# Performance work log

Measured on AMD Instinct MI355X. Metric: run time of the kernel, lower is better.

## Reference

```python
import jax, jax.numpy as jnp
import numpy as np

TOPK = 13
NUM_CLASSES = 80
ALPHA = 1.0
BETA = 6.0
EPS = 1e-9
IMG = 640.0


def setup_inputs() -> dict:
    key = jax.random.key(0)
    k = jax.random.split(key, 8)
    bs, A, C, n = 32, 8400, NUM_CLASSES, 64
    pd_scores = jax.random.uniform(k[0], (bs, A, C), dtype=jnp.float32)
    # valid x1y1x2y2 predicted boxes
    ctr = jax.random.uniform(k[1], (bs, A, 2), dtype=jnp.float32) * IMG
    wh = jax.random.uniform(k[2], (bs, A, 2), dtype=jnp.float32) * 90.0 + 10.0
    pd_bboxes = jnp.concatenate([ctr - wh / 2, ctr + wh / 2], axis=-1)
    anc_points = jax.random.uniform(k[3], (8400, 2), dtype=jnp.float32) * IMG
    gt_labels = jax.random.randint(k[4], (bs, n, 1), 0, C, dtype=jnp.int64)
    gctr = jax.random.uniform(k[5], (bs, n, 2), dtype=jnp.float32) * IMG
    gwh = jax.random.uniform(k[6], (bs, n, 2), dtype=jnp.float32) * 140.0 + 20.0
    gt_bboxes = jnp.concatenate([gctr - gwh / 2, gctr + gwh / 2], axis=-1)
    mask_gt = (jax.random.uniform(k[7], (bs, n, 1)) < 0.8).astype(jnp.float32)
    return {"pd_scores": pd_scores, "pd_bboxes": pd_bboxes, "anc_points": anc_points,
            "gt_labels": gt_labels, "gt_bboxes": gt_bboxes, "mask_gt": mask_gt}


def _assign(pd_scores, pd_bboxes, anc_points, gt_labels, gt_bboxes, mask_gt):
    b, A, C = pd_scores.shape
    n = gt_bboxes.shape[1]
    gl = gt_labels.reshape(b, n).astype(jnp.int32)

    # bbox_scores[b,n,a] = pd_scores[b, a, gt_labels[b,n]]  -> (b, n, A)
    bbox_scores = jnp.take_along_axis(pd_scores.transpose(0, 2, 1), gl[:, :, None], axis=1)

    # pairwise IoU: gt (b,n,1,4) vs pred (b,1,A,4) -> (b,n,A)
    b1 = gt_bboxes[:, :, None, :]
    b2 = pd_bboxes[:, None, :, :]
    lt = jnp.maximum(b1[..., :2], b2[..., :2])
    rb = jnp.minimum(b1[..., 2:], b2[..., 2:])
    overlap = jnp.clip(rb - lt, 0).prod(-1)
    area1 = jnp.clip(b1[..., 2:] - b1[..., :2], 0).prod(-1)
    area2 = jnp.clip(b2[..., 2:] - b2[..., :2], 0).prod(-1)
    overlaps = overlap / (area1 + area2 - overlap + EPS)

    align_metric = (bbox_scores ** ALPHA) * (overlaps ** BETA)

    # anchor centers inside gt boxes -> (b,n,A)
    lt_d = anc_points[None, None, :, :] - gt_bboxes[:, :, None, :2]
    rb_d = gt_bboxes[:, :, None, 2:] - anc_points[None, None, :, :]
    deltas = jnp.concatenate([lt_d, rb_d], axis=-1)
    mask_in_gts = (deltas.min(-1) > EPS).astype(gt_bboxes.dtype)

    # topk candidate selection with scatter-count (avoids (b,n,topk,A) one-hot)
    metrics = align_metric * mask_in_gts
    _, topk_idxs = jax.lax.top_k(metrics, TOPK)  # (b,n,TOPK)
    topk_mask = mask_gt.reshape(b, n, 1) != 0
    topk_idxs = jnp.where(topk_mask, topk_idxs, 0)
    bi = jnp.arange(b)[:, None, None]
    ni = jnp.arange(n)[None, :, None]
    counts = jnp.zeros((b, n, A), jnp.int32).at[bi, ni, topk_idxs].add(1)
    is_in_topk = jnp.where(counts > 1, 0, counts).astype(metrics.dtype)

    mask_pos = is_in_topk * mask_in_gts * mask_gt.reshape(b, n, 1)

    # resolve anchors assigned to multiple gts by highest IoU
    fg_mask = mask_pos.sum(-2)                         # (b,A)
    mask_multi = fg_mask[:, None, :] > 1               # (b,1,A) broadcast over n
    max_idx = overlaps.argmax(axis=1)                  # (b,A)
    is_max = jax.nn.one_hot(max_idx, n, dtype=overlaps.dtype).transpose(0, 2, 1)  # (b,n,A)
    mask_pos = jnp.where(mask_multi, is_max, mask_pos)
    fg_mask = mask_pos.sum(-2)
    target_gt_idx = mask_pos.argmax(-2)                # (b,A)

    # gather targets
    target_labels = jnp.take_along_axis(gl, target_gt_idx, axis=1)            # (b,A)
    target_labels = jnp.maximum(target_labels, 0)
    target_bboxes = jnp.take_along_axis(gt_bboxes, target_gt_idx[:, :, None], axis=1)  # (b,A,4)
    target_scores = jax.nn.one_hot(target_labels, C, dtype=pd_scores.dtype)
    target_scores = jnp.where(fg_mask[:, :, None] > 0, target_scores, 0.0)

    # normalize scores by alignment metric
    align_metric = align_metric * mask_pos
    pos_align = align_metric.max(-1, keepdims=True)                  # (b,n,1)
    pos_overlaps = (overlaps * mask_pos).max(-1, keepdims=True)      # (b,n,1)
    norm = (align_metric * pos_overlaps / (pos_align + EPS)).max(-2)[:, :, None]  # (b,A,1)
    target_scores = target_scores * norm

    return target_labels, target_bboxes, target_scores, fg_mask > 0


def reference(pd_scores, pd_bboxes, anc_points, gt_labels, gt_bboxes, mask_gt):
    return _assign(pd_scores, pd_bboxes, anc_points, gt_labels, gt_bboxes, mask_gt)
```

## Files before the change

### kernel.cpp

```cpp
#include <hip/hip_runtime.h>
#include <math.h>

#define A_N   8400
#define BS    32
#define NGT   64
#define NC    80
#define TK    13
#define EPSF  1e-9f
#define CAP   1024
#define JG    32
#define NJG   2
#define NTILE 33
#define PCAP  64

typedef float nt4 __attribute__((ext_vector_type(4)));

#define OFF_LB 0
#define OFF_BB (BS * A_N)
#define OFF_SC (OFF_BB + BS * A_N * 4)
#define OFF_FG (OFF_SC + BS * A_N * NC)

#define WS_FLAG   0
#define WS_CNT    256
#define WS_MINJ   (WS_CNT   + BS * A_N * 4)
#define WS_INFO   (WS_MINJ  + BS * A_N * 4)
#define WS_ALIGN  (WS_INFO  + BS * A_N * 4)
#define WS_POSA   (WS_ALIGN + BS * A_N * 4)
#define WS_POSO   (WS_POSA  + BS * NGT * 4)
#define WS_CNT2   (WS_POSO  + BS * NGT * 4)
#define WS_CAND   (WS_CNT2  + BS * NGT * 4)

__device__ __forceinline__ float iou_f(float g0, float g1, float g2, float g3,
                                       float p0, float p1, float p2, float p3) {
    float ltx = fmaxf(g0, p0), lty = fmaxf(g1, p1);
    float rbx = fminf(g2, p2), rby = fminf(g3, p3);
    float ov  = fmaxf(rbx - ltx, 0.f) * fmaxf(rby - lty, 0.f);
    float a1  = fmaxf(g2 - g0, 0.f) * fmaxf(g3 - g1, 0.f);
    float a2  = fmaxf(p2 - p0, 0.f) * fmaxf(p3 - p1, 0.f);
    return ov / (a1 + a2 - ov + EPSF);
}

__device__ __forceinline__ int get_gl(const int* g, int flag64, int i) {
    return flag64 ? g[2 * i] : g[i];
}

__device__ __forceinline__ unsigned long long shfl_xor_u64(unsigned long long x, int m) {
    int lo = __shfl_xor((int)(unsigned int)(x & 0xFFFFFFFFull), m, 64);
    int hi = __shfl_xor((int)(unsigned int)(x >> 32), m, 64);
    return ((unsigned long long)(unsigned int)hi << 32) | (unsigned int)lo;
}

__global__ __launch_bounds__(256) void k_init(int* cnt, int* minj,
                                              unsigned int* posA, unsigned int* posO,
                                              int* cnt2, int* flag, const int* gl_raw) {
    int i = blockIdx.x * 256 + threadIdx.x;
    if (i < BS * A_N) { cnt[i] = 0; minj[i] = 1 << 30; }
    if (i < BS * NGT) { posA[i] = 0u; posO[i] = 0u; cnt2[i] = 0; }
    if (i == 0) {
        int f = 1;
        for (int k = 0; k < 64; k++) {
            if (gl_raw[2 * k + 1] != 0) { f = 0; break; }
        }
        *flag = f;
    }
}

__global__ __launch_bounds__(256) void k_cand(
    const float* __restrict__ pd_scores, const float* __restrict__ pd_bboxes,
    const float* __restrict__ anc, const int* __restrict__ gl_raw,
    const float* __restrict__ gt_bboxes, const float* __restrict__ mask_gt,
    const int* __restrict__ flag,
    int* __restrict__ cnt2, unsigned long long* __restrict__ cand) {
    __shared__ float4 sgt[JG];
    __shared__ int    slbl[JG];
    __shared__ int    smask[JG];
    __shared__ int    cnt_lds[JG];
    __shared__ int    base_lds[JG];
    __shared__ unsigned long long pool[JG][PCAP];

    int bid  = blockIdx.x;
    int b    = bid / (NTILE * NJG);
    int rem  = bid % (NTILE * NJG);
    int tile = rem / NJG;
    int jg   = rem % NJG;
    int tid  = threadIdx.x;
    int a    = tile * 256 + tid;
    int jbase = b * NGT + jg * JG;

    if (tid < JG) {
        sgt[tid]   = ((const float4*)gt_bboxes)[jbase + tid];
        slbl[tid]  = get_gl(gl_raw, *flag, jbase + tid);
        smask[tid] = (mask_gt[jbase + tid] != 0.f);
        cnt_lds[tid] = 0;
    }
    __syncthreads();

    bool act = (a < A_N);
    float2 an = make_float2(0.f, 0.f);
    float4 p  = make_float4(0.f, 0.f, 0.f, 0.f);
    const float* sc = pd_scores;
    if (act) {
        an = ((const float2*)anc)[a];
        p  = ((const float4*)pd_bboxes)[(size_t)b * A_N + a];
        sc = pd_scores + (size_t)b * A_N * NC + (size_t)a * NC;
    }

    for (int j = 0; j < JG; j++) {
        if (!smask[j]) continue;
        if (!act) continue;
        float4 g = sgt[j];
        float d = fminf(fminf(an.x - g.x, an.y - g.y),
                        fminf(g.z - an.x, g.w - an.y));
        if (d > EPSF) {
            float iou = iou_f(g.x, g.y, g.z, g.w, p.x, p.y, p.z, p.w);
            float m = 0.f;
            if (iou > 0.f) {
                float s = sc[slbl[j]];
                m = s * powf(iou, 6.0f);
            }
            unsigned long long key =
                ((unsigned long long)__float_as_uint(m) << 32) |
                (unsigned int)(~(unsigned int)a);
            int slot = atomicAdd(&cnt_lds[j], 1);
            if (slot < PCAP) {
                pool[j][slot] = key;
            } else {
                int gs = atomicAdd(&cnt2[jbase + j], 1);
                if (gs < CAP) cand[(size_t)(jbase + j) * CAP + gs] = key;
            }
        }
    }
    __syncthreads();

    if (tid < JG) {
        int c = min(cnt_lds[tid], PCAP);
        int bas = 0;
        if (c > 0) bas = atomicAdd(&cnt2[jbase + tid], c);
        base_lds[tid] = bas;
    }
    __syncthreads();

    for (int j = 0; j < JG; j++) {
        int c = min(cnt_lds[j], PCAP);
        int bas = base_lds[j];
        for (int t = tid; t < c; t += 256) {
            int dst = bas + t;
            if (dst < CAP) cand[(size_t)(jbase + j) * CAP + dst] = pool[j][t];
        }
    }
}

__global__ __launch_bounds__(256) void k_pick(
    const int* __restrict__ cnt2, const unsigned long long* __restrict__ cand,
    int* __restrict__ cnt, int* __restrict__ minj) {
    int lane = threadIdx.x & 63;
    int wave = threadIdx.x >> 6;
    int bj = blockIdx.x * 4 + wave;
    int b = bj >> 6, j = bj & 63;

    int n = min(cnt2[bj], CAP);
    if (n == 0) return;

    const unsigned long long* L = cand + (size_t)bj * CAP;
    unsigned long long k0[CAP / 64];
    #pragma unroll
    for (int t = 0; t < CAP / 64; t++) {
        int i = t * 64 + lane;
        k0[t] = (i < n) ? L[i] : 0ULL;
    }

    unsigned int wanchor[TK];
    int P = 0;
    #pragma unroll
    for (int r = 0; r < TK; r++) {
        unsigned long long best = 0;
        #pragma unroll
        for (int t = 0; t < CAP / 64; t++) best = (k0[t] > best) ? k0[t] : best;
        for (int s = 1; s < 64; s <<= 1) {
            unsigned long long o = shfl_xor_u64(best, s);
            if (o > best) best = o;
        }
        if (!(best >> 32)) break;
        unsigned int aw = ~(unsigned int)(best & 0xFFFFFFFFull);
        wanchor[r] = aw;
        if (lane == 0) {
            atomicAdd(&cnt[b * A_N + (int)aw], 1);
            atomicMin(&minj[b * A_N + (int)aw], j);
        }
        #pragma unroll
        for (int t = 0; t < CAP / 64; t++) if (k0[t] == best) k0[t] = 0;
        P++;
    }

    if (P < TK) {
        int K = TK - P;
        #pragma unroll
        for (int t = 0; t < CAP / 64; t++) {
            unsigned long long key = k0[t];
            if (key != 0 && !(key >> 32)) {
                unsigned int a0 = ~(unsigned int)(key & 0xFFFFFFFFull);
                int off = 0;
                #pragma unroll
                for (int r = 0; r < TK; r++)
                    if (r < P && wanchor[r] < a0) off++;
                if ((int)a0 < K + off) {
                    atomicAdd(&cnt[b * A_N + (int)a0], 1);
                    atomicMin(&minj[b * A_N + (int)a0], j);
                }
            }
        }
    }
}

__global__ __launch_bounds__(256) void k_assign(
    const float* __restrict__ pd_scores, const float* __restrict__ pd_bboxes,
    const float* __restrict__ gt_bboxes, const int* __restrict__ gl_raw,
    const int* __restrict__ flag,
    const int* __restrict__ cnt, const int* __restrict__ minj,
    int* __restrict__ info, float* __restrict__ alignArr,
    unsigned int* posA, unsigned int* posO, float* __restrict__ out) {
    int i = blockIdx.x * 256 + threadIdx.x;
    if (i >= BS * A_N) return;
    int b = i / A_N;
    int c = cnt[i];
    int f64 = *flag;

    float4 p = ((const float4*)pd_bboxes)[i];
    int jstar = 0;
    if (c == 1) {
        jstar = minj[i];
    } else if (c > 1) {
        float bv = -1.f; int bj_ = 0;
        const float4* gb = (const float4*)(gt_bboxes + (size_t)b * NGT * 4);
        for (int j = 0; j < NGT; j++) {
            float4 g = gb[j];
            float ov = iou_f(g.x, g.y, g.z, g.w, p.x, p.y, p.z, p.w);
            if (ov > bv) { bv = ov; bj_ = j; }
        }
        jstar = bj_;
    }

    int lbl = get_gl(gl_raw, f64, b * NGT + jstar);
    if (lbl < 0) lbl = 0;

    out[OFF_LB + i] = (float)lbl;
    float4 g = ((const float4*)gt_bboxes)[b * NGT + jstar];
    ((float4*)(out + OFF_BB))[i] = g;

    int fg = (c > 0) ? 1 : 0;
    out[OFF_FG + i] = (float)fg;

    float al = 0.f;
    if (fg) {
        float ov = iou_f(g.x, g.y, g.z, g.w, p.x, p.y, p.z, p.w);
        float s  = pd_scores[(size_t)i * NC + lbl];
        al = s * powf(ov, 6.0f);
        atomicMax((int*)&posA[b * NGT + jstar], __float_as_int(al));
        atomicMax((int*)&posO[b * NGT + jstar], __float_as_int(ov));
    }
    alignArr[i] = al;
    info[i] = jstar | (lbl << 8) | (fg << 16);
}

__global__ __launch_bounds__(256) void k_scores(
    const int* __restrict__ info, const float* __restrict__ alignArr,
    const unsigned int* __restrict__ posA, const unsigned int* __restrict__ posO,
    float* __restrict__ out) {
    int t = blockIdx.x * 256 + threadIdx.x;
    const int TOT = BS * A_N * (NC / 4);
    if (t >= TOT) return;
    int anchor = t / (NC / 4);
    int q = t - anchor * (NC / 4);
    int inf = info[anchor];
    nt4 v = (nt4)(0.f);
    if (inf & (1 << 16)) {
        int lbl = (inf >> 8) & 255;
        int c0 = q * 4;
        if (lbl >= c0 && lbl < c0 + 4) {
            int jstar = inf & 255;
            int b = anchor / A_N;
            float pa = __int_as_float((int)posA[b * NGT + jstar]);
            float po = __int_as_float((int)posO[b * NGT + jstar]);
            float norm = alignArr[anchor] * po / (pa + EPSF);
            v[lbl - c0] = norm;
        }
    }
    __builtin_nontemporal_store(v, &((nt4*)(out + OFF_SC))[t]);
}

extern "C" void kernel_launch(void* const* d_in, const int* in_sizes, int n_in,
                              void* d_out, int out_size, void* d_ws, size_t ws_size,
                              hipStream_t stream) {
    const float* pd_scores = (const float*)d_in[0];
    const float* pd_bboxes = (const float*)d_in[1];
    const float* anc       = (const float*)d_in[2];
    const int*   gl_raw    = (const int*)d_in[3];
    const float* gt_bboxes = (const float*)d_in[4];
    const float* mask_gt   = (const float*)d_in[5];
    float* out = (float*)d_out;

    char* ws = (char*)d_ws;
    int*                flag     = (int*)(ws + WS_FLAG);
    int*                cnt      = (int*)(ws + WS_CNT);
    int*                minj     = (int*)(ws + WS_MINJ);
    int*                info     = (int*)(ws + WS_INFO);
    float*              alignArr = (float*)(ws + WS_ALIGN);
    unsigned int*       posA     = (unsigned int*)(ws + WS_POSA);
    unsigned int*       posO     = (unsigned int*)(ws + WS_POSO);
    int*                cnt2     = (int*)(ws + WS_CNT2);
    unsigned long long* cand     = (unsigned long long*)(ws + WS_CAND);

    k_init<<<(BS * A_N + 255) / 256, 256, 0, stream>>>(cnt, minj, posA, posO, cnt2, flag, gl_raw);
    k_cand<<<BS * NTILE * NJG, 256, 0, stream>>>(pd_scores, pd_bboxes, anc, gl_raw,
                                                 gt_bboxes, mask_gt, flag, cnt2, cand);
    k_pick<<<BS * NGT / 4, 256, 0, stream>>>(cnt2, cand, cnt, minj);
    k_assign<<<(BS * A_N + 255) / 256, 256, 0, stream>>>(pd_scores, pd_bboxes, gt_bboxes,
                                                         gl_raw, flag, cnt, minj,
                                                         info, alignArr, posA, posO, out);
    k_scores<<<(BS * A_N * (NC / 4) + 255) / 256, 256, 0, stream>>>(info, alignArr,
                                                                    posA, posO, out);
}
```

Baseline: 217.3 us.

## Zero score output inside candidate kernel and scatter only positive norms

The dense zero fill of the score output and the cnt/minj initialisation move into k_cand as grid-stride loops, so they overlap with the candidate computation and k_init shrinks to a tiny launch. The final kernel now writes a single scalar per foreground anchor instead of rewriting the whole 80-class row. This removes a full pass that read info per vec4 and wrote the dense score tensor. In exchange k_cand carries extra store traffic, and the ordering between the zero fill and the later scattered writes relies on kernel boundaries.

Measured after the change: 215.7 us. About the same (-0.8%).

```diff
diff --git a/kernel.cpp b/kernel.cpp
--- a/kernel.cpp
+++ b/kernel.cpp
@@ -12,6 +12,7 @@
 #define NJG   2
 #define NTILE 33
 #define PCAP  64
+#define NCAND (BS * NTILE * NJG)
 
 typedef float nt4 __attribute__((ext_vector_type(4)));
 
@@ -50,11 +51,9 @@
     return ((unsigned long long)(unsigned int)hi << 32) | (unsigned int)lo;
 }
 
-__global__ __launch_bounds__(256) void k_init(int* cnt, int* minj,
-                                              unsigned int* posA, unsigned int* posO,
+__global__ __launch_bounds__(256) void k_init(unsigned int* posA, unsigned int* posO,
                                               int* cnt2, int* flag, const int* gl_raw) {
     int i = blockIdx.x * 256 + threadIdx.x;
-    if (i < BS * A_N) { cnt[i] = 0; minj[i] = 1 << 30; }
     if (i < BS * NGT) { posA[i] = 0u; posO[i] = 0u; cnt2[i] = 0; }
     if (i == 0) {
         int f = 1;
@@ -70,7 +69,8 @@
     const float* __restrict__ anc, const int* __restrict__ gl_raw,
     const float* __restrict__ gt_bboxes, const float* __restrict__ mask_gt,
     const int* __restrict__ flag,
-    int* __restrict__ cnt2, unsigned long long* __restrict__ cand) {
+    int* __restrict__ cnt2, unsigned long long* __restrict__ cand,
+    int* __restrict__ cnt, int* __restrict__ minj, float* __restrict__ out) {
     __shared__ float4 sgt[JG];
     __shared__ int    slbl[JG];
     __shared__ int    smask[JG];
@@ -92,6 +92,17 @@
         slbl[tid]  = get_gl(gl_raw, *flag, jbase + tid);
         smask[tid] = (mask_gt[jbase + tid] != 0.f);
         cnt_lds[tid] = 0;
+    }
+
+    {
+        int gth = bid * 256 + tid;
+        const int GS = NCAND * 256;
+        nt4* scz = (nt4*)(out + OFF_SC);
+        for (int t = gth; t < BS * A_N * (NC / 4); t += GS)
+            __builtin_nontemporal_store((nt4)(0.f), &scz[t]);
+        for (int t = gth; t < BS * A_N; t += GS) {
+            cnt[t] = 0; minj[t] = 1 << 30;
+        }
     }
     __syncthreads();
 
@@ -262,30 +273,20 @@
     info[i] = jstar | (lbl << 8) | (fg << 16);
 }
 
-__global__ __launch_bounds__(256) void k_scores(
+__global__ __launch_bounds__(256) void k_norm(
     const int* __restrict__ info, const float* __restrict__ alignArr,
     const unsigned int* __restrict__ posA, const unsigned int* __restrict__ posO,
     float* __restrict__ out) {
-    int t = blockIdx.x * 256 + threadIdx.x;
-    const int TOT = BS * A_N * (NC / 4);
-    if (t >= TOT) return;
-    int anchor = t / (NC / 4);
-    int q = t - anchor * (NC / 4);
-    int inf = info[anchor];
-    nt4 v = (nt4)(0.f);
-    if (inf & (1 << 16)) {
-        int lbl = (inf >> 8) & 255;
-        int c0 = q * 4;
-        if (lbl >= c0 && lbl < c0 + 4) {
-            int jstar = inf & 255;
-            int b = anchor / A_N;
-            float pa = __int_as_float((int)posA[b * NGT + jstar]);
-            float po = __int_as_float((int)posO[b * NGT + jstar]);
-            float norm = alignArr[anchor] * po / (pa + EPSF);
-            v[lbl - c0] = norm;
-        }
-    }
-    __builtin_nontemporal_store(v, &((nt4*)(out + OFF_SC))[t]);
+    int i = blockIdx.x * 256 + threadIdx.x;
+    if (i >= BS * A_N) return;
+    int inf = info[i];
+    if (!(inf & (1 << 16))) return;
+    int jstar = inf & 255;
+    int lbl   = (inf >> 8) & 255;
+    int b = i / A_N;
+    float pa = __int_as_float((int)posA[b * NGT + jstar]);
+    float po = __int_as_float((int)posO[b * NGT + jstar]);
+    out[OFF_SC + (size_t)i * NC + lbl] = alignArr[i] * po / (pa + EPSF);
 }
 
 extern "C" void kernel_launch(void* const* d_in, const int* in_sizes, int n_in,
@@ -310,13 +311,13 @@
     int*                cnt2     = (int*)(ws + WS_CNT2);
     unsigned long long* cand     = (unsigned long long*)(ws + WS_CAND);
 
-    k_init<<<(BS * A_N + 255) / 256, 256, 0, stream>>>(cnt, minj, posA, posO, cnt2, flag, gl_raw);
-    k_cand<<<BS * NTILE * NJG, 256, 0, stream>>>(pd_scores, pd_bboxes, anc, gl_raw,
-                                                 gt_bboxes, mask_gt, flag, cnt2, cand);
+    k_init<<<8, 256, 0, stream>>>(posA, posO, cnt2, flag, gl_raw);
+    k_cand<<<NCAND, 256, 0, stream>>>(pd_scores, pd_bboxes, anc, gl_raw,
+                                      gt_bboxes, mask_gt, flag, cnt2, cand,
+                                      cnt, minj, out);
     k_pick<<<BS * NGT / 4, 256, 0, stream>>>(cnt2, cand, cnt, minj);
     k_assign<<<(BS * A_N + 255) / 256, 256, 0, stream>>>(pd_scores, pd_bboxes, gt_bboxes,
                                                          gl_raw, flag, cnt, minj,
                                                          info, alignArr, posA, posO, out);
-    k_scores<<<(BS * A_N * (NC / 4) + 255) / 256, 256, 0, stream>>>(info, alignArr,
-                                                                    posA, posO, out);
-}
+    k_norm<<<(BS * A_N + 255) / 256, 256, 0, stream>>>(info, alignArr, posA, posO, out);
+}
```
